# Performance work log

Measured on AMD Instinct MI355X. Metric: run time of the kernel, lower is better.

The kernel has to match this reference:

```python
import jax, jax.numpy as jnp
import numpy as np
from jax.scipy.ndimage import map_coordinates

# Geometry (parallel-beam analogue of the astra projector in the source)
NUMPIX = 256          # image is NUMPIX x NUMPIX
NUMBIN = 367          # detector bins (~ NUMPIX*sqrt(2), 1-pixel spacing)
NUMTHETA = 360        # projection angles over [0, 360) deg
NS = 4                # number of ordered subsets (angles j::NS per subset)
NT = 367              # samples along each ray (covers image diagonal)
BETA = 1.0            # relaxation parameter
DX = 1.0              # pixel size
THRESHOLD = 0.01      # IterativeLayer residual threshold
MAX_ITERS = 2         # IterativeLayer max_iterations
EPS = float(np.finfo(np.float64).eps)
DEN_EPS = 1e-6        # guard for Minv/Dinv denominators

_theta = np.deg2rad(np.arange(NUMTHETA) * (360.0 / NUMTHETA)).astype(np.float32)
_COS = jnp.asarray(np.cos(_theta), dtype=jnp.float32)
_SIN = jnp.asarray(np.sin(_theta), dtype=jnp.float32)
_CDET = (NUMBIN - 1) / 2.0
_CPIX = (NUMPIX - 1) / 2.0
_S = jnp.arange(NUMBIN, dtype=jnp.float32) - _CDET          # detector coords
_T = jnp.arange(NT, dtype=jnp.float32) - (NT - 1) / 2.0     # along-ray coords
_pix = jnp.arange(NUMPIX, dtype=jnp.float32) - _CPIX
_Y, _X = jnp.meshgrid(_pix, _pix, indexing='ij')            # pixel centers


def forward_project(f, ca, sa):
    # Radon transform of f for angles (ca, sa): line integral along each ray.
    # coords: [na, NUMBIN, NT]
    x = _S[None, :, None] * ca[:, None, None] - _T[None, None, :] * sa[:, None, None]
    y = _S[None, :, None] * sa[:, None, None] + _T[None, None, :] * ca[:, None, None]
    vals = map_coordinates(f, [y + _CPIX, x + _CPIX], order=1, mode='constant', cval=0.0)
    return vals.sum(-1)  # [na, NUMBIN]


def backproject(g, ca, sa):
    # Adjoint-style backprojection of sinogram g [na, NUMBIN] onto the image grid.
    def one(ga, c, s_):
        sd = _X * c + _Y * s_ + _CDET                      # [NUMPIX, NUMPIX]
        i0 = jnp.floor(sd)
        w = sd - i0
        i0i = i0.astype(jnp.int32)
        v0 = jnp.where((i0i >= 0) & (i0i < NUMBIN), ga[jnp.clip(i0i, 0, NUMBIN - 1)], 0.0)
        i1i = i0i + 1
        v1 = jnp.where((i1i >= 0) & (i1i < NUMBIN), ga[jnp.clip(i1i, 0, NUMBIN - 1)], 0.0)
        return v0 * (1.0 - w) + v1 * w
    return jax.vmap(one)(g, ca, sa).sum(0)


def sart_reconstruct(f, sino):
    # Precompute SART normalizers per subset: Minv = A_j(1_img), Dinv = A_j^T(1_sino).
    cas = [_COS[j::NS] for j in range(NS)]
    sas = [_SIN[j::NS] for j in range(NS)]
    ones_img = jnp.ones((NUMPIX, NUMPIX), dtype=f.dtype)
    Minv = [jnp.maximum(forward_project(ones_img, cas[j], sas[j]), DEN_EPS) for j in range(NS)]
    Dinv = [jnp.maximum(backproject(jnp.ones_like(sino[j::NS]), cas[j], sas[j]), DEN_EPS) for j in range(NS)]

    for _ in range(MAX_ITERS):
        # inner denoiser layer modeled as identity
        fk = f
        for j in range(NS):  # one SART ordered-subset sweep
            fp = forward_project(fk, cas[j], sas[j])
            diffs = (sino[j::NS] - fp * DX) / Minv[j] / DX
            bp = backproject(diffs, cas[j], sas[j])
            bp = jnp.where(jnp.abs(bp) > 1000.0, 0.0, bp)
            fk = fk + BETA * bp / Dinv[j]
        fk = jnp.maximum(fk, EPS)
        # residual ||A fk * dx - sino||_F, computed subset-by-subset
        res2 = jnp.float32(0.0)
        for j in range(NS):
            fpj = forward_project(fk, cas[j], sas[j])
            res2 = res2 + jnp.sum((fpj * DX - sino[j::NS]) ** 2)
        res = jnp.sqrt(res2)
        f = jnp.where(res > THRESHOLD, fk, f)
    return f


def setup_inputs() -> dict:
    key = jax.random.key(0)
    k1, k2 = jax.random.split(key)
    f0 = jax.random.uniform(k1, (NUMPIX, NUMPIX), dtype=jnp.float32)
    sino = jax.random.uniform(k2, (NUMTHETA, NUMBIN), dtype=jnp.float32)
    return {"f0": f0, "sino": sino}


def reference(f0, sino):
    return sart_reconstruct(f0, sino)
```

## Files before the change

### kernel.cpp

```cpp
#include <hip/hip_runtime.h>
#include <math.h>

#define NUMPIX 256
#define NUMBIN 367
#define NUMTHETA 360
#define NS 4
#define NT 367
#define NPIX2 (NUMPIX * NUMPIX)
#define NRAYS_ALL (NUMTHETA * NUMBIN)
#define NANG_SUB (NUMTHETA / NS)
#define NRAYS_SUB (NANG_SUB * NUMBIN)

#define NANG_HALF 180
#define NRAYS_HALF (NANG_HALF * NUMBIN)
#define NANG_SUBH (NANG_SUB / 2)
#define NRAYS_SUBH (NANG_SUBH * NUMBIN)

#define CDET 183.0f
#define CPIX 127.5f
#define TOFF 183.0f
#define DEN_EPS 1e-6f
#define EPS_F 2.2204460492503131e-16f
#define RES2_THRESH 1e-4f
#define INV_DINV (1.0f / 90.0f)

#define QW 260
#define QROWS 258
#define QN2 (QW * QROWS)
#define QNF (QN2 * 2)

#define HALF_BLOCKS ((NRAYS_HALF + 15) / 16)
#define SUBH_BLOCKS ((NRAYS_SUBH + 15) / 16)

typedef float f4q __attribute__((ext_vector_type(4), aligned(8)));
typedef float f2u __attribute__((ext_vector_type(2), aligned(4)));

#define OFF_COS   0
#define OFF_SIN   (OFF_COS + NUMTHETA)
#define OFF_MINV  (OFF_SIN + NUMTHETA)
#define OFF_Q     (OFF_MINV + NRAYS_ALL + 8)
#define OFF_QT    (OFF_Q + QNF)
#define OFF_DIFF  (OFF_QT + QNF)

__device__ __forceinline__ void clip_axis2(float c0, float rate,
                                           float bLo, float bHi,
                                           float& lo, float& hi) {
    if (fabsf(rate) > 1e-6f) {
        float inv = 1.0f / rate;
        float a = (bLo - c0) * inv;
        float b = (bHi - c0) * inv;
        lo = fmaxf(lo, fminf(a, b));
        hi = fminf(hi, fmaxf(a, b));
    } else if (c0 <= bLo || c0 >= bHi) {
        lo = 1e9f; hi = -1e9f;
    }
}

__device__ __forceinline__ int ray_chunks16(float x0, float y0, float ca, float sa,
                                            int& itlo) {
    float lo = -1e9f, hi = 1e9f;
    clip_axis2(x0, -sa, -2.0f, 257.0f, lo, hi);
    clip_axis2(y0,  ca, -2.0f, 257.0f, lo, hi);
    if (hi < lo) { itlo = 0; return 0; }
    int a = (int)floorf(lo + TOFF) - 1; if (a < 0) a = 0;
    int b = (int)ceilf(hi + TOFF) + 1;  if (b > NT - 1) b = NT - 1;
    itlo = a;
    if (b < a) return 0;
    return (b - a + 16) >> 4;
}

__global__ __launch_bounds__(256)
void init_minv_kernel(float* __restrict__ cosA, float* __restrict__ sinA,
                      float* __restrict__ Qf, float* __restrict__ QTf,
                      float* __restrict__ fcur, float* __restrict__ minv,
                      const float* __restrict__ f0) {
    int idx = blockIdx.x * blockDim.x + threadIdx.x;
    if (idx < NUMTHETA) {
        float th = (float)((double)idx * 0.017453292519943295);
        cosA[idx] = (float)cos((double)th);
        sinA[idx] = (float)sin((double)th);
    }
    if (idx < NPIX2) fcur[idx] = f0[idx];
    if (idx < QN2) {
        int qr = idx / QW, qc = idx - qr * QW;
        int r = qr - 1, c = qc - 1;
        bool cv = ((unsigned)c < 256u);
        bool rv0 = ((unsigned)r < 256u), rv1 = ((unsigned)(r + 1) < 256u);
        float a = (cv && rv0) ? f0[r * NUMPIX + c] : 0.0f;
        float b = (cv && rv1) ? f0[(r + 1) * NUMPIX + c] : 0.0f;
        Qf[idx * 2] = a;  Qf[idx * 2 + 1] = b;
        float ta = (cv && rv0) ? f0[c * NUMPIX + r] : 0.0f;
        float tb = (cv && rv1) ? f0[c * NUMPIX + (r + 1)] : 0.0f;
        QTf[idx * 2] = ta;  QTf[idx * 2 + 1] = tb;
    }

    const int lane = threadIdx.x & 63;
    const int wid = threadIdx.x >> 6;
    const int sub = lane >> 4, slane = lane & 15;
    int ray = blockIdx.x * 16 + wid * 4 + sub;
    if (ray >= NRAYS_HALF) return;
    int angle = ray / NUMBIN;
    int bin = ray - angle * NUMBIN;
    float th = (float)((double)angle * 0.017453292519943295);
    float ca, sa;
    __sincosf(th, &sa, &ca);
    float s = (float)bin - CDET;
    float x0 = fmaf(s, ca, CPIX);
    float y0 = fmaf(s, sa, CPIX);
    float acc = 0.0f;
    int count = 0;
    float lo = -1e9f, hi = 1e9f;
    clip_axis2(x0, -sa, -2.0f, 257.0f, lo, hi);
    clip_axis2(y0,  ca, -2.0f, 257.0f, lo, hi);
    int e1a = 0, e1b = -1, e2a = 0, e2b = -1;
    if (hi >= lo) {
        int itA = (int)floorf(lo + TOFF) - 1; if (itA < 0) itA = 0;
        int itB = (int)ceilf(hi + TOFF) + 1;  if (itB > NT - 1) itB = NT - 1;
        if (itB >= itA) {
            float ilo = -1e9f, ihi = 1e9f;
            clip_axis2(x0, -sa, 0.05f, 254.95f, ilo, ihi);
            clip_axis2(y0,  ca, 0.05f, 254.95f, ilo, ihi);
            int jA = 1, jB = 0;
            if (ihi >= ilo) {
                jA = (int)ceilf(ilo + TOFF) + 1;
                jB = (int)floorf(ihi + TOFF) - 1;
                if (jA < itA) jA = itA;
                if (jB > itB) jB = itB;
            }
            if (jB >= jA) {
                count = jB - jA + 1;
                e1a = itA; e1b = jA - 1;
                e2a = jB + 1; e2b = itB;
            } else {
                e1a = itA; e1b = itB;
            }
        }
    }
    #pragma unroll 1
    for (int base = e1a; base <= e1b; base += 16) {
        int t = base + slane;
        float tt = (float)t - TOFF;
        float x = fmaf(-tt, sa, x0);
        float y = fmaf(tt, ca, y0);
        float fx = floorf(x), fy = floorf(y);
        float wx = x - fx, wy = y - fy;
        int c0 = (int)fx, r0 = (int)fy;
        float ux = (((unsigned)c0 < 256u) ? (1.0f - wx) : 0.0f) +
                   (((unsigned)(c0 + 1) < 256u) ? wx : 0.0f);
        float uy = (((unsigned)r0 < 256u) ? (1.0f - wy) : 0.0f) +
                   (((unsigned)(r0 + 1) < 256u) ? wy : 0.0f);
        if (t <= e1b) acc += ux * uy;
    }
    #pragma unroll 1
    for (int base = e2a; base <= e2b; base += 16) {
        int t = base + slane;
        float tt = (float)t - TOFF;
        float x = fmaf(-tt, sa, x0);
        float y = fmaf(tt, ca, y0);
        float fx = floorf(x), fy = floorf(y);
        float wx = x - fx, wy = y - fy;
        int c0 = (int)fx, r0 = (int)fy;
        float ux = (((unsigned)c0 < 256u) ? (1.0f - wx) : 0.0f) +
                   (((unsigned)(c0 + 1) < 256u) ? wx : 0.0f);
        float uy = (((unsigned)r0 < 256u) ? (1.0f - wy) : 0.0f) +
                   (((unsigned)(r0 + 1) < 256u) ? wy : 0.0f);
        if (t <= e2b) acc += ux * uy;
    }
    acc += __shfl_down(acc, 8, 16);
    acc += __shfl_down(acc, 4, 16);
    acc += __shfl_down(acc, 2, 16);
    acc += __shfl_down(acc, 1, 16);
    if (slane == 0) {
        float m = fmaxf(acc + (float)count, DEN_EPS);
        minv[angle * NUMBIN + bin] = m;
        minv[(angle + NANG_HALF) * NUMBIN + (NUMBIN - 1 - bin)] = m;
    }
}

template <int MODE>
__global__ __launch_bounds__(256)
void fp_kernel(const float* __restrict__ Qn,
               const float* __restrict__ Qt,
               const float* __restrict__ sino,
               const float* __restrict__ minv,
               float* __restrict__ out,
               const float* __restrict__ cosA,
               const float* __restrict__ sinA,
               int angleStart, int angleStride, int nRays) {
    const int wid = threadIdx.x >> 6, lane = threadIdx.x & 63;
    const int sub = lane >> 4, slane = lane & 15;

    int ray = (blockIdx.x * 4 + wid) * 4 + sub;
    bool valid = ray < nRays;
    int rr = valid ? ray : nRays - 1;
    int ai = rr / NUMBIN;
    int bin = rr - ai * NUMBIN;
    int angle = angleStart + ai * angleStride;
    float ca = cosA[angle], sa = sinA[angle];
    float s = (float)bin - CDET;
    float x0 = fmaf(s, ca, CPIX);
    float y0 = fmaf(s, sa, CPIX);
    int itlo, nc = ray_chunks16(x0, y0, ca, sa, itlo);
    if (!valid) nc = 0;

    bool useT = fabsf(ca) > fabsf(sa);
    const float* img = (useT ? Qt : Qn) + (QW + 1) * 2;
    float u0 = useT ? y0 : x0, du = useT ? ca : -sa;
    float v0 = useT ? x0 : y0, dv = useT ? -sa : ca;

    float tt0 = (float)(itlo + slane) - TOFF;
    float u = fmaf(tt0, du, u0);
    float v = fmaf(tt0, dv, v0);
    const float du16 = du * 16.0f, dv16 = dv * 16.0f;
    const float du32 = du * 32.0f, dv32 = dv * 32.0f;

    float acc0 = 0.0f, acc1 = 0.0f;
    int ic = 0;
    for (; ic + 1 < nc; ic += 2) {
        float uA = fminf(fmaxf(u, -1.0f), 256.0f);
        float vA = fminf(fmaxf(v, -1.0f), 256.0f);
        float uB = fminf(fmaxf(u + du16, -1.0f), 256.0f);
        float vB = fminf(fmaxf(v + dv16, -1.0f), 256.0f);
        float fuA = floorf(uA), fvA = floorf(vA);
        float fuB = floorf(uB), fvB = floorf(vB);
        float wuA = uA - fuA, wvA = vA - fvA;
        float wuB = uB - fuB, wvB = vB - fvB;
        int idxA = (int)fmaf(fvA, (float)QW, fuA);
        int idxB = (int)fmaf(fvB, (float)QW, fuB);
        f4q qA = *(const f4q*)(img + idxA * 2);
        f4q qB = *(const f4q*)(img + idxB * 2);
        float topA = fmaf(wuA, qA.z - qA.x, qA.x);
        float botA = fmaf(wuA, qA.w - qA.y, qA.y);
        acc0 += fmaf(wvA, botA - topA, topA);
        float topB = fmaf(wuB, qB.z - qB.x, qB.x);
        float botB = fmaf(wuB, qB.w - qB.y, qB.y);
        acc1 += fmaf(wvB, botB - topB, topB);
        u += du32; v += dv32;
    }
    if (ic < nc) {
        float uc = fminf(fmaxf(u, -1.0f), 256.0f);
        float vc = fminf(fmaxf(v, -1.0f), 256.0f);
        float fu = floorf(uc), fv = floorf(vc);
        float wu = uc - fu, wv = vc - fv;
        int idx = (int)fmaf(fv, (float)QW, fu);
        f4q q = *(const f4q*)(img + idx * 2);
        float top = fmaf(wu, q.z - q.x, q.x);
        float bot = fmaf(wu, q.w - q.y, q.y);
        acc0 += fmaf(wv, bot - top, top);
    }
    float acc = acc0 + acc1;
    acc += __shfl_down(acc, 8, 16);
    acc += __shfl_down(acc, 4, 16);
    acc += __shfl_down(acc, 2, 16);
    acc += __shfl_down(acc, 1, 16);

    if (MODE == 1) {
        if (slane == 0 && valid) {
            out[ai * NUMBIN + bin] =
                (sino[angle * NUMBIN + bin] - acc) /
                minv[angle * NUMBIN + bin];
            int a2 = angle + NANG_HALF;
            int b2 = NUMBIN - 1 - bin;
            out[(ai + NANG_SUBH) * NUMBIN + b2] =
                (sino[a2 * NUMBIN + b2] - acc) /
                minv[a2 * NUMBIN + b2];
        }
    } else {
        float d2 = 0.0f;
        if (slane == 0 && valid) {
            float d = acc - sino[angle * NUMBIN + bin];
            int a2 = angle + NANG_HALF;
            int b2 = NUMBIN - 1 - bin;
            float dm = acc - sino[a2 * NUMBIN + b2];
            d2 = d * d + dm * dm;
        }
        d2 += __shfl_down(d2, 16);
        d2 += __shfl_down(d2, 32);
        __shared__ float part[4];
        if (lane == 0) part[wid] = d2;
        __syncthreads();
        if (threadIdx.x == 0)
            out[blockIdx.x] = part[0] + part[1] + part[2] + part[3];
    }
}

__global__ __launch_bounds__(256)
void bp_update_kernel(float* __restrict__ Qf,
                      float* __restrict__ QTf,
                      const float* __restrict__ g,
                      const float* __restrict__ cosA,
                      const float* __restrict__ sinA,
                      int j, int doClamp) {
    __shared__ float part[4][64];
    const int tx = threadIdx.x & 63;
    const int ty = threadIdx.x >> 6;
    int p = blockIdx.x * 64 + tx;
    int px = p & (NUMPIX - 1), py = p >> 8;
    float X = (float)px - CPIX, Y = (float)py - CPIX;
    float acc = 0.0f;
    for (int i = ty; i < NANG_SUB; i += 4) {
        int angle = j + NS * i;
        float ca = cosA[angle], sa = sinA[angle];
        float sd = fmaf(X, ca, fmaf(Y, sa, CDET));
        float f0 = floorf(sd);
        float w = sd - f0;
        int i0 = (int)f0;
        f2u gv = *(const f2u*)(g + i * NUMBIN + i0);
        acc += fmaf(w, gv.y - gv.x, gv.x);
    }
    part[ty][tx] = acc;
    __syncthreads();
    if (ty == 0) {
        float s = part[0][tx] + part[1][tx] + part[2][tx] + part[3][tx];
        float bp = (fabsf(s) > 1000.0f) ? 0.0f : s;
        float v = Qf[((py + 1) * QW + (px + 1)) * 2] + bp * INV_DINV;
        if (doClamp) v = fmaxf(v, EPS_F);
        Qf[((py + 1) * QW + (px + 1)) * 2]      = v;
        Qf[(py * QW + (px + 1)) * 2 + 1]        = v;
        QTf[((px + 1) * QW + (py + 1)) * 2]     = v;
        QTf[(px * QW + (py + 1)) * 2 + 1]       = v;
    }
}

__global__ __launch_bounds__(256)
void select_kernel(float* __restrict__ fcur,
                   float* __restrict__ Qf, float* __restrict__ QTf,
                   const float* __restrict__ part, int last) {
    __shared__ float buf[4];
    const int tid = threadIdx.x;
    float a = 0.0f;
    for (int idx = tid; idx < HALF_BLOCKS; idx += 256) a += part[idx];
    #pragma unroll
    for (int off = 32; off; off >>= 1) a += __shfl_down(a, off);
    if ((tid & 63) == 0) buf[tid >> 6] = a;
    __syncthreads();
    float tot = buf[0] + buf[1] + buf[2] + buf[3];
    bool upd = (tot > RES2_THRESH);
    int p = blockIdx.x * 256 + tid;
    int px = p & (NUMPIX - 1), py = p >> 8;
    float v = upd ? Qf[((py + 1) * QW + (px + 1)) * 2] : fcur[p];
    fcur[p] = v;
    if (!last) {
        Qf[((py + 1) * QW + (px + 1)) * 2]      = v;
        Qf[(py * QW + (px + 1)) * 2 + 1]        = v;
        QTf[((px + 1) * QW + (py + 1)) * 2]     = v;
        QTf[(px * QW + (py + 1)) * 2 + 1]       = v;
    }
}

extern "C" void kernel_launch(void* const* d_in, const int* in_sizes, int n_in,
                              void* d_out, int out_size, void* d_ws, size_t ws_size,
                              hipStream_t stream) {
    const float* f0 = (const float*)d_in[0];
    const float* sino = (const float*)d_in[1];
    float* fcur = (float*)d_out;
    float* ws = (float*)d_ws;

    float* cosA = ws + OFF_COS;
    float* sinA = ws + OFF_SIN;
    float* minv = ws + OFF_MINV;
    float* Qf   = ws + OFF_Q;
    float* QTf  = ws + OFF_QT;
    float* diff = ws + OFF_DIFF;

    init_minv_kernel<<<HALF_BLOCKS, 256, 0, stream>>>(
        cosA, sinA, Qf, QTf, fcur, minv, f0);

    for (int iter = 0; iter < 2; iter++) {
        for (int j = 0; j < NS; j++) {
            fp_kernel<1><<<SUBH_BLOCKS, 256, 0, stream>>>(
                Qf, QTf, sino, minv, diff, cosA, sinA, j, NS, NRAYS_SUBH);
            bp_update_kernel<<<NPIX2 / 64, 256, 0, stream>>>(
                Qf, QTf, diff, cosA, sinA, j, (j == NS - 1) ? 1 : 0);
        }
        fp_kernel<2><<<HALF_BLOCKS, 256, 0, stream>>>(
            Qf, QTf, sino, nullptr, diff, cosA, sinA, 0, 1, NRAYS_HALF);
        select_kernel<<<NPIX2 / 256, 256, 0, stream>>>(
            fcur, Qf, QTf, diff, iter == 1);
    }
}
```

Baseline: 257.9 us.

## Speculate second-iteration first subset against both candidates, merge residual into one launch

The first residual forward projection is fused into a single launch with the second iteration's first-subset projection. That projection is computed speculatively from both the updated image and the original f0 copy, and the backprojection picks one from the residual flag read on the device. The select kernel is removed, and the final residual and output selection move into a last-block-done reduction with atomics. Backprojection also uses the half-angle symmetry to read mirrored diffs. This trades extra Q0 buffers and doubled gathers in the merged kernel for fewer launches and serial stages.

```diff
diff --git a/kernel.cpp b/kernel.cpp
--- a/kernel.cpp
+++ b/kernel.cpp
@@ -38,9 +38,13 @@
 #define OFF_COS   0
 #define OFF_SIN   (OFF_COS + NUMTHETA)
 #define OFF_MINV  (OFF_SIN + NUMTHETA)
-#define OFF_Q     (OFF_MINV + NRAYS_ALL + 8)
+#define OFF_RES   (OFF_MINV + NRAYS_ALL)
+#define OFF_Q     (OFF_RES + 8)
 #define OFF_QT    (OFF_Q + QNF)
-#define OFF_DIFF  (OFF_QT + QNF)
+#define OFF_Q0    (OFF_QT + QNF)
+#define OFF_QT0   (OFF_Q0 + QNF)
+#define OFF_DIFF  (OFF_QT0 + QNF)
+#define OFF_DIFFB (OFF_DIFF + NRAYS_SUB + 2)
 
 __device__ __forceinline__ void clip_axis2(float c0, float rate,
                                            float bLo, float bHi,
@@ -69,10 +73,102 @@
     return (b - a + 16) >> 4;
 }
 
+struct RaySetup {
+    int angle, bin, ai, nc;
+    float u, v, du, dv;
+    bool useT;
+};
+
+__device__ __forceinline__ RaySetup ray_setup(int rr, int angleStart, int angleStride,
+                                              const float* __restrict__ cosA,
+                                              const float* __restrict__ sinA,
+                                              int slane) {
+    RaySetup R;
+    R.ai = rr / NUMBIN;
+    R.bin = rr - R.ai * NUMBIN;
+    R.angle = angleStart + R.ai * angleStride;
+    float ca = cosA[R.angle], sa = sinA[R.angle];
+    float s = (float)R.bin - CDET;
+    float x0 = fmaf(s, ca, CPIX);
+    float y0 = fmaf(s, sa, CPIX);
+    int itlo;
+    R.nc = ray_chunks16(x0, y0, ca, sa, itlo);
+    R.useT = fabsf(ca) > fabsf(sa);
+    float u0 = R.useT ? y0 : x0, du = R.useT ? ca : -sa;
+    float v0 = R.useT ? x0 : y0, dv = R.useT ? -sa : ca;
+    float tt0 = (float)(itlo + slane) - TOFF;
+    R.u = fmaf(tt0, du, u0);
+    R.v = fmaf(tt0, dv, v0);
+    R.du = du; R.dv = dv;
+    return R;
+}
+
+template <bool DUAL>
+__device__ __forceinline__ void march(const float* __restrict__ imgA,
+                                      const float* __restrict__ imgB,
+                                      float u, float v, float du, float dv,
+                                      int nc, float& outA, float& outB) {
+    const float du16 = du * 16.0f, dv16 = dv * 16.0f;
+    const float du32 = du * 32.0f, dv32 = dv * 32.0f;
+    float a0 = 0.0f, a1 = 0.0f, b0 = 0.0f, b1 = 0.0f;
+    int ic = 0;
+    for (; ic + 1 < nc; ic += 2) {
+        float u1 = fminf(fmaxf(u, -1.0f), 256.0f);
+        float v1 = fminf(fmaxf(v, -1.0f), 256.0f);
+        float u2 = fminf(fmaxf(u + du16, -1.0f), 256.0f);
+        float v2 = fminf(fmaxf(v + dv16, -1.0f), 256.0f);
+        float fu1 = floorf(u1), fv1 = floorf(v1);
+        float fu2 = floorf(u2), fv2 = floorf(v2);
+        float wu1 = u1 - fu1, wv1 = v1 - fv1;
+        float wu2 = u2 - fu2, wv2 = v2 - fv2;
+        int idx1 = (int)fmaf(fv1, (float)QW, fu1);
+        int idx2 = (int)fmaf(fv2, (float)QW, fu2);
+        f4q qa1 = *(const f4q*)(imgA + idx1 * 2);
+        f4q qa2 = *(const f4q*)(imgA + idx2 * 2);
+        float t1 = fmaf(wu1, qa1.z - qa1.x, qa1.x);
+        float c1 = fmaf(wu1, qa1.w - qa1.y, qa1.y);
+        a0 += fmaf(wv1, c1 - t1, t1);
+        float t2 = fmaf(wu2, qa2.z - qa2.x, qa2.x);
+        float c2 = fmaf(wu2, qa2.w - qa2.y, qa2.y);
+        a1 += fmaf(wv2, c2 - t2, t2);
+        if (DUAL) {
+            f4q qb1 = *(const f4q*)(imgB + idx1 * 2);
+            f4q qb2 = *(const f4q*)(imgB + idx2 * 2);
+            float s1 = fmaf(wu1, qb1.z - qb1.x, qb1.x);
+            float d1 = fmaf(wu1, qb1.w - qb1.y, qb1.y);
+            b0 += fmaf(wv1, d1 - s1, s1);
+            float s2 = fmaf(wu2, qb2.z - qb2.x, qb2.x);
+            float d2 = fmaf(wu2, qb2.w - qb2.y, qb2.y);
+            b1 += fmaf(wv2, d2 - s2, s2);
+        }
+        u += du32; v += dv32;
+    }
+    if (ic < nc) {
+        float u1 = fminf(fmaxf(u, -1.0f), 256.0f);
+        float v1 = fminf(fmaxf(v, -1.0f), 256.0f);
+        float fu1 = floorf(u1), fv1 = floorf(v1);
+        float wu1 = u1 - fu1, wv1 = v1 - fv1;
+        int idx1 = (int)fmaf(fv1, (float)QW, fu1);
+        f4q qa1 = *(const f4q*)(imgA + idx1 * 2);
+        float t1 = fmaf(wu1, qa1.z - qa1.x, qa1.x);
+        float c1 = fmaf(wu1, qa1.w - qa1.y, qa1.y);
+        a0 += fmaf(wv1, c1 - t1, t1);
+        if (DUAL) {
+            f4q qb1 = *(const f4q*)(imgB + idx1 * 2);
+            float s1 = fmaf(wu1, qb1.z - qb1.x, qb1.x);
+            float d1 = fmaf(wu1, qb1.w - qb1.y, qb1.y);
+            b0 += fmaf(wv1, d1 - s1, s1);
+        }
+    }
+    outA = a0 + a1;
+    outB = b0 + b1;
+}
+
 __global__ __launch_bounds__(256)
 void init_minv_kernel(float* __restrict__ cosA, float* __restrict__ sinA,
                       float* __restrict__ Qf, float* __restrict__ QTf,
-                      float* __restrict__ fcur, float* __restrict__ minv,
+                      float* __restrict__ Q0f, float* __restrict__ QT0f,
+                      float* __restrict__ minv,
                       const float* __restrict__ f0) {
     int idx = blockIdx.x * blockDim.x + threadIdx.x;
     if (idx < NUMTHETA) {
@@ -80,7 +176,6 @@
         cosA[idx] = (float)cos((double)th);
         sinA[idx] = (float)sin((double)th);
     }
-    if (idx < NPIX2) fcur[idx] = f0[idx];
     if (idx < QN2) {
         int qr = idx / QW, qc = idx - qr * QW;
         int r = qr - 1, c = qc - 1;
@@ -89,9 +184,11 @@
         float a = (cv && rv0) ? f0[r * NUMPIX + c] : 0.0f;
         float b = (cv && rv1) ? f0[(r + 1) * NUMPIX + c] : 0.0f;
         Qf[idx * 2] = a;  Qf[idx * 2 + 1] = b;
+        Q0f[idx * 2] = a; Q0f[idx * 2 + 1] = b;
         float ta = (cv && rv0) ? f0[c * NUMPIX + r] : 0.0f;
         float tb = (cv && rv1) ? f0[c * NUMPIX + (r + 1)] : 0.0f;
         QTf[idx * 2] = ta;  QTf[idx * 2 + 1] = tb;
+        QT0f[idx * 2] = ta; QT0f[idx * 2 + 1] = tb;
     }
 
     const int lane = threadIdx.x & 63;
@@ -177,174 +274,198 @@
     }
 }
 
-template <int MODE>
-__global__ __launch_bounds__(256)
-void fp_kernel(const float* __restrict__ Qn,
-               const float* __restrict__ Qt,
-               const float* __restrict__ sino,
-               const float* __restrict__ minv,
-               float* __restrict__ out,
-               const float* __restrict__ cosA,
-               const float* __restrict__ sinA,
-               int angleStart, int angleStride, int nRays) {
+__device__ __forceinline__ float res_block_partial(
+        int unit, const float* __restrict__ Qn, const float* __restrict__ Qt,
+        const float* __restrict__ sino,
+        const float* __restrict__ cosA, const float* __restrict__ sinA,
+        float* partLds) {
     const int wid = threadIdx.x >> 6, lane = threadIdx.x & 63;
     const int sub = lane >> 4, slane = lane & 15;
-
-    int ray = (blockIdx.x * 4 + wid) * 4 + sub;
-    bool valid = ray < nRays;
-    int rr = valid ? ray : nRays - 1;
-    int ai = rr / NUMBIN;
-    int bin = rr - ai * NUMBIN;
-    int angle = angleStart + ai * angleStride;
-    float ca = cosA[angle], sa = sinA[angle];
-    float s = (float)bin - CDET;
-    float x0 = fmaf(s, ca, CPIX);
-    float y0 = fmaf(s, sa, CPIX);
-    int itlo, nc = ray_chunks16(x0, y0, ca, sa, itlo);
-    if (!valid) nc = 0;
-
-    bool useT = fabsf(ca) > fabsf(sa);
-    const float* img = (useT ? Qt : Qn) + (QW + 1) * 2;
-    float u0 = useT ? y0 : x0, du = useT ? ca : -sa;
-    float v0 = useT ? x0 : y0, dv = useT ? -sa : ca;
-
-    float tt0 = (float)(itlo + slane) - TOFF;
-    float u = fmaf(tt0, du, u0);
-    float v = fmaf(tt0, dv, v0);
-    const float du16 = du * 16.0f, dv16 = dv * 16.0f;
-    const float du32 = du * 32.0f, dv32 = dv * 32.0f;
-
-    float acc0 = 0.0f, acc1 = 0.0f;
-    int ic = 0;
-    for (; ic + 1 < nc; ic += 2) {
-        float uA = fminf(fmaxf(u, -1.0f), 256.0f);
-        float vA = fminf(fmaxf(v, -1.0f), 256.0f);
-        float uB = fminf(fmaxf(u + du16, -1.0f), 256.0f);
-        float vB = fminf(fmaxf(v + dv16, -1.0f), 256.0f);
-        float fuA = floorf(uA), fvA = floorf(vA);
-        float fuB = floorf(uB), fvB = floorf(vB);
-        float wuA = uA - fuA, wvA = vA - fvA;
-        float wuB = uB - fuB, wvB = vB - fvB;
-        int idxA = (int)fmaf(fvA, (float)QW, fuA);
-        int idxB = (int)fmaf(fvB, (float)QW, fuB);
-        f4q qA = *(const f4q*)(img + idxA * 2);
-        f4q qB = *(const f4q*)(img + idxB * 2);
-        float topA = fmaf(wuA, qA.z - qA.x, qA.x);
-        float botA = fmaf(wuA, qA.w - qA.y, qA.y);
-        acc0 += fmaf(wvA, botA - topA, topA);
-        float topB = fmaf(wuB, qB.z - qB.x, qB.x);
-        float botB = fmaf(wuB, qB.w - qB.y, qB.y);
-        acc1 += fmaf(wvB, botB - topB, topB);
-        u += du32; v += dv32;
-    }
-    if (ic < nc) {
-        float uc = fminf(fmaxf(u, -1.0f), 256.0f);
-        float vc = fminf(fmaxf(v, -1.0f), 256.0f);
-        float fu = floorf(uc), fv = floorf(vc);
-        float wu = uc - fu, wv = vc - fv;
-        int idx = (int)fmaf(fv, (float)QW, fu);
-        f4q q = *(const f4q*)(img + idx * 2);
-        float top = fmaf(wu, q.z - q.x, q.x);
-        float bot = fmaf(wu, q.w - q.y, q.y);
-        acc0 += fmaf(wv, bot - top, top);
-    }
-    float acc = acc0 + acc1;
+    int ray = unit * 16 + wid * 4 + sub;
+    bool valid = ray < NRAYS_HALF;
+    int rr = valid ? ray : NRAYS_HALF - 1;
+    RaySetup R = ray_setup(rr, 0, 1, cosA, sinA, slane);
+    const float* img = (R.useT ? Qt : Qn) + (QW + 1) * 2;
+    float acc, dum;
+    march<false>(img, img, R.u, R.v, R.du, R.dv, valid ? R.nc : 0, acc, dum);
     acc += __shfl_down(acc, 8, 16);
     acc += __shfl_down(acc, 4, 16);
     acc += __shfl_down(acc, 2, 16);
     acc += __shfl_down(acc, 1, 16);
-
-    if (MODE == 1) {
-        if (slane == 0 && valid) {
-            out[ai * NUMBIN + bin] =
-                (sino[angle * NUMBIN + bin] - acc) /
-                minv[angle * NUMBIN + bin];
-            int a2 = angle + NANG_HALF;
-            int b2 = NUMBIN - 1 - bin;
-            out[(ai + NANG_SUBH) * NUMBIN + b2] =
-                (sino[a2 * NUMBIN + b2] - acc) /
-                minv[a2 * NUMBIN + b2];
+    float d2 = 0.0f;
+    if (slane == 0 && valid) {
+        float d = acc - sino[R.angle * NUMBIN + R.bin];
+        int a2 = R.angle + NANG_HALF;
+        int b2 = NUMBIN - 1 - R.bin;
+        float dm = acc - sino[a2 * NUMBIN + b2];
+        d2 = d * d + dm * dm;
+    }
+    d2 += __shfl_down(d2, 16);
+    d2 += __shfl_down(d2, 32);
+    if (lane == 0) partLds[wid] = d2;
+    __syncthreads();
+    return partLds[0] + partLds[1] + partLds[2] + partLds[3];
+}
+
+__global__ __launch_bounds__(256)
+void fp_sub_kernel(const float* __restrict__ Qn, const float* __restrict__ Qt,
+                   const float* __restrict__ sino, const float* __restrict__ minv,
+                   float* __restrict__ gOut,
+                   const float* __restrict__ cosA, const float* __restrict__ sinA,
+                   int j) {
+    const int wid = threadIdx.x >> 6, lane = threadIdx.x & 63;
+    const int sub = lane >> 4, slane = lane & 15;
+    int ray = blockIdx.x * 16 + wid * 4 + sub;
+    bool valid = ray < NRAYS_SUBH;
+    int rr = valid ? ray : NRAYS_SUBH - 1;
+    RaySetup R = ray_setup(rr, j, NS, cosA, sinA, slane);
+    const float* img = (R.useT ? Qt : Qn) + (QW + 1) * 2;
+    float acc, dum;
+    march<false>(img, img, R.u, R.v, R.du, R.dv, valid ? R.nc : 0, acc, dum);
+    acc += __shfl_down(acc, 8, 16);
+    acc += __shfl_down(acc, 4, 16);
+    acc += __shfl_down(acc, 2, 16);
+    acc += __shfl_down(acc, 1, 16);
+    if (slane == 0 && valid) {
+        gOut[R.ai * NUMBIN + R.bin] =
+            (sino[R.angle * NUMBIN + R.bin] - acc) /
+            minv[R.angle * NUMBIN + R.bin];
+        int a2 = R.angle + NANG_HALF;
+        int b2 = NUMBIN - 1 - R.bin;
+        gOut[(R.ai + NANG_SUBH) * NUMBIN + b2] =
+            (sino[a2 * NUMBIN + b2] - acc) /
+            minv[a2 * NUMBIN + b2];
+    }
+}
+
+__global__ __launch_bounds__(256)
+void fp_merged_kernel(const float* __restrict__ Qn, const float* __restrict__ Qt,
+                      const float* __restrict__ Q0n, const float* __restrict__ Q0t,
+                      const float* __restrict__ sino, const float* __restrict__ minv,
+                      float* __restrict__ gA, float* __restrict__ gB,
+                      const float* __restrict__ cosA, const float* __restrict__ sinA,
+                      float* __restrict__ resbuf) {
+    __shared__ float part[4];
+    int bid = blockIdx.x;
+    if (bid < HALF_BLOCKS) {
+        float tot = res_block_partial(bid, Qn, Qt, sino, cosA, sinA, part);
+        if (threadIdx.x == 0) atomicAdd(&resbuf[0], tot);
+        return;
+    }
+    int bid2 = bid - HALF_BLOCKS;
+    const int wid = threadIdx.x >> 6, lane = threadIdx.x & 63;
+    const int sub = lane >> 4, slane = lane & 15;
+    int ray = bid2 * 16 + wid * 4 + sub;
+    bool valid = ray < NRAYS_SUBH;
+    int rr = valid ? ray : NRAYS_SUBH - 1;
+    RaySetup R = ray_setup(rr, 0, NS, cosA, sinA, slane);
+    const float* imgA = (R.useT ? Qt : Qn) + (QW + 1) * 2;
+    const float* imgB = (R.useT ? Q0t : Q0n) + (QW + 1) * 2;
+    float accA, accB;
+    march<true>(imgA, imgB, R.u, R.v, R.du, R.dv, valid ? R.nc : 0, accA, accB);
+    accA += __shfl_down(accA, 8, 16);
+    accB += __shfl_down(accB, 8, 16);
+    accA += __shfl_down(accA, 4, 16);
+    accB += __shfl_down(accB, 4, 16);
+    accA += __shfl_down(accA, 2, 16);
+    accB += __shfl_down(accB, 2, 16);
+    accA += __shfl_down(accA, 1, 16);
+    accB += __shfl_down(accB, 1, 16);
+    if (slane == 0 && valid) {
+        float m1 = minv[R.angle * NUMBIN + R.bin];
+        float s1 = sino[R.angle * NUMBIN + R.bin];
+        gA[R.ai * NUMBIN + R.bin] = (s1 - accA) / m1;
+        gB[R.ai * NUMBIN + R.bin] = (s1 - accB) / m1;
+        int a2 = R.angle + NANG_HALF;
+        int b2 = NUMBIN - 1 - R.bin;
+        float m2 = minv[a2 * NUMBIN + b2];
+        float s2 = sino[a2 * NUMBIN + b2];
+        gA[(R.ai + NANG_SUBH) * NUMBIN + b2] = (s2 - accA) / m2;
+        gB[(R.ai + NANG_SUBH) * NUMBIN + b2] = (s2 - accB) / m2;
+    }
+}
+
+__global__ __launch_bounds__(256)
+void fp_final_kernel(const float* __restrict__ Qn, const float* __restrict__ Qt,
+                     const float* __restrict__ sino,
+                     const float* __restrict__ cosA, const float* __restrict__ sinA,
+                     float* __restrict__ resbuf,
+                     float* __restrict__ fcur, const float* __restrict__ f0) {
+    __shared__ float part[4];
+    __shared__ int lastFlag;
+    float tot = res_block_partial(blockIdx.x, Qn, Qt, sino, cosA, sinA, part);
+    if (threadIdx.x == 0) {
+        atomicAdd(&resbuf[1], tot);
+        __threadfence();
+        unsigned old = atomicAdd((unsigned*)resbuf + 2, 1u);
+        lastFlag = (old == (unsigned)(gridDim.x - 1)) ? 1 : 0;
+    }
+    __syncthreads();
+    if (!lastFlag) return;
+    float r2 = atomicAdd(&resbuf[1], 0.0f);
+    float r1 = atomicAdd(&resbuf[0], 0.0f);
+    bool upd2 = r2 > RES2_THRESH;
+    bool upd1 = r1 > RES2_THRESH;
+    const int tid = threadIdx.x;
+    #pragma unroll 4
+    for (int p = tid; p < NPIX2; p += 256) {
+        int px = p & (NUMPIX - 1), py = p >> 8;
+        float v = upd2 ? Qn[((py + 1) * QW + (px + 1)) * 2]
+                       : (upd1 ? fcur[p] : f0[p]);
+        fcur[p] = v;
+    }
+}
+
+__global__ __launch_bounds__(256)
+void bp_update_kernel(float* __restrict__ Qf, float* __restrict__ QTf,
+                      const float* __restrict__ Q0f,
+                      const float* __restrict__ gA, const float* __restrict__ gB,
+                      const float* __restrict__ cosA, const float* __restrict__ sinA,
+                      float* __restrict__ resbuf, float* __restrict__ fcur,
+                      int j, int doClamp, int writeFcur, int chooseFlag,
+                      int zeroSel) {
+    __shared__ float part[4][64];
+    if (zeroSel && blockIdx.x == 0 && threadIdx.x == 0) {
+        if (zeroSel == 1) {
+            resbuf[0] = 0.0f;
+        } else {
+            resbuf[1] = 0.0f;
+            ((unsigned*)resbuf)[2] = 0u;
         }
-    } else {
-        float d2 = 0.0f;
-        if (slane == 0 && valid) {
-            float d = acc - sino[angle * NUMBIN + bin];
-            int a2 = angle + NANG_HALF;
-            int b2 = NUMBIN - 1 - bin;
-            float dm = acc - sino[a2 * NUMBIN + b2];
-            d2 = d * d + dm * dm;
-        }
-        d2 += __shfl_down(d2, 16);
-        d2 += __shfl_down(d2, 32);
-        __shared__ float part[4];
-        if (lane == 0) part[wid] = d2;
-        __syncthreads();
-        if (threadIdx.x == 0)
-            out[blockIdx.x] = part[0] + part[1] + part[2] + part[3];
-    }
-}
-
-__global__ __launch_bounds__(256)
-void bp_update_kernel(float* __restrict__ Qf,
-                      float* __restrict__ QTf,
-                      const float* __restrict__ g,
-                      const float* __restrict__ cosA,
-                      const float* __restrict__ sinA,
-                      int j, int doClamp) {
-    __shared__ float part[4][64];
+    }
+    const float* g = gA;
+    const float* src = Qf;
+    if (chooseFlag && !(resbuf[0] > RES2_THRESH)) { g = gB; src = Q0f; }
     const int tx = threadIdx.x & 63;
     const int ty = threadIdx.x >> 6;
     int p = blockIdx.x * 64 + tx;
     int px = p & (NUMPIX - 1), py = p >> 8;
     float X = (float)px - CPIX, Y = (float)py - CPIX;
     float acc = 0.0f;
-    for (int i = ty; i < NANG_SUB; i += 4) {
+    for (int i = ty; i < NANG_SUBH; i += 4) {
         int angle = j + NS * i;
         float ca = cosA[angle], sa = sinA[angle];
         float sd = fmaf(X, ca, fmaf(Y, sa, CDET));
-        float f0 = floorf(sd);
-        float w = sd - f0;
-        int i0 = (int)f0;
+        float fl = floorf(sd);
+        float w = sd - fl;
+        int i0 = (int)fl;
         f2u gv = *(const f2u*)(g + i * NUMBIN + i0);
         acc += fmaf(w, gv.y - gv.x, gv.x);
+        f2u gw = *(const f2u*)(g + (i + NANG_SUBH) * NUMBIN + (365 - i0));
+        acc += fmaf(w, gw.x - gw.y, gw.y);
     }
     part[ty][tx] = acc;
     __syncthreads();
     if (ty == 0) {
         float s = part[0][tx] + part[1][tx] + part[2][tx] + part[3][tx];
         float bp = (fabsf(s) > 1000.0f) ? 0.0f : s;
-        float v = Qf[((py + 1) * QW + (px + 1)) * 2] + bp * INV_DINV;
+        float v = src[((py + 1) * QW + (px + 1)) * 2] + bp * INV_DINV;
         if (doClamp) v = fmaxf(v, EPS_F);
         Qf[((py + 1) * QW + (px + 1)) * 2]      = v;
         Qf[(py * QW + (px + 1)) * 2 + 1]        = v;
         QTf[((px + 1) * QW + (py + 1)) * 2]     = v;
         QTf[(px * QW + (py + 1)) * 2 + 1]       = v;
-    }
-}
-
-__global__ __launch_bounds__(256)
-void select_kernel(float* __restrict__ fcur,
-                   float* __restrict__ Qf, float* __restrict__ QTf,
-                   const float* __restrict__ part, int last) {
-    __shared__ float buf[4];
-    const int tid = threadIdx.x;
-    float a = 0.0f;
-    for (int idx = tid; idx < HALF_BLOCKS; idx += 256) a += part[idx];
-    #pragma unroll
-    for (int off = 32; off; off >>= 1) a += __shfl_down(a, off);
-    if ((tid & 63) == 0) buf[tid >> 6] = a;
-    __syncthreads();
-    float tot = buf[0] + buf[1] + buf[2] + buf[3];
-    bool upd = (tot > RES2_THRESH);
-    int p = blockIdx.x * 256 + tid;
-    int px = p & (NUMPIX - 1), py = p >> 8;
-    float v = upd ? Qf[((py + 1) * QW + (px + 1)) * 2] : fcur[p];
-    fcur[p] = v;
-    if (!last) {
-        Qf[((py + 1) * QW + (px + 1)) * 2]      = v;
-        Qf[(py * QW + (px + 1)) * 2 + 1]        = v;
-        QTf[((px + 1) * QW + (py + 1)) * 2]     = v;
-        QTf[(px * QW + (py + 1)) * 2 + 1]       = v;
+        if (writeFcur) fcur[p] = v;
     }
 }
 
@@ -359,23 +480,38 @@
     float* cosA = ws + OFF_COS;
     float* sinA = ws + OFF_SIN;
     float* minv = ws + OFF_MINV;
+    float* resb = ws + OFF_RES;
     float* Qf   = ws + OFF_Q;
     float* QTf  = ws + OFF_QT;
-    float* diff = ws + OFF_DIFF;
+    float* Q0f  = ws + OFF_Q0;
+    float* QT0f = ws + OFF_QT0;
+    float* dfA  = ws + OFF_DIFF;
+    float* dfB  = ws + OFF_DIFFB;
 
     init_minv_kernel<<<HALF_BLOCKS, 256, 0, stream>>>(
-        cosA, sinA, Qf, QTf, fcur, minv, f0);
-
-    for (int iter = 0; iter < 2; iter++) {
-        for (int j = 0; j < NS; j++) {
-            fp_kernel<1><<<SUBH_BLOCKS, 256, 0, stream>>>(
-                Qf, QTf, sino, minv, diff, cosA, sinA, j, NS, NRAYS_SUBH);
-            bp_update_kernel<<<NPIX2 / 64, 256, 0, stream>>>(
-                Qf, QTf, diff, cosA, sinA, j, (j == NS - 1) ? 1 : 0);
-        }
-        fp_kernel<2><<<HALF_BLOCKS, 256, 0, stream>>>(
-            Qf, QTf, sino, nullptr, diff, cosA, sinA, 0, 1, NRAYS_HALF);
-        select_kernel<<<NPIX2 / 256, 256, 0, stream>>>(
-            fcur, Qf, QTf, diff, iter == 1);
-    }
-}
+        cosA, sinA, Qf, QTf, Q0f, QT0f, minv, f0);
+
+    for (int j = 0; j < NS; j++) {
+        fp_sub_kernel<<<SUBH_BLOCKS, 256, 0, stream>>>(
+            Qf, QTf, sino, minv, dfA, cosA, sinA, j);
+        bp_update_kernel<<<NPIX2 / 64, 256, 0, stream>>>(
+            Qf, QTf, Q0f, dfA, dfB, cosA, sinA, resb, fcur,
+            j, (j == NS - 1) ? 1 : 0, (j == NS - 1) ? 1 : 0, 0,
+            (j == NS - 1) ? 1 : 0);
+    }
+    fp_merged_kernel<<<HALF_BLOCKS + SUBH_BLOCKS, 256, 0, stream>>>(
+        Qf, QTf, Q0f, QT0f, sino, minv, dfA, dfB, cosA, sinA, resb);
+    bp_update_kernel<<<NPIX2 / 64, 256, 0, stream>>>(
+        Qf, QTf, Q0f, dfA, dfB, cosA, sinA, resb, fcur,
+        0, 0, 0, 1, 0);
+    for (int j = 1; j < NS; j++) {
+        fp_sub_kernel<<<SUBH_BLOCKS, 256, 0, stream>>>(
+            Qf, QTf, sino, minv, dfA, cosA, sinA, j);
+        bp_update_kernel<<<NPIX2 / 64, 256, 0, stream>>>(
+            Qf, QTf, Q0f, dfA, dfB, cosA, sinA, resb, fcur,
+            j, (j == NS - 1) ? 1 : 0, 0, 0,
+            (j == NS - 1) ? 2 : 0);
+    }
+    fp_final_kernel<<<HALF_BLOCKS, 256, 0, stream>>>(
+        Qf, QTf, sino, cosA, sinA, resb, fcur, f0);
+}
```

After: 438.8 us. 70.1% more time.
